# Performance work log

Hardware: AMD Instinct MI355X
Metric: run time of the kernel (lower is better)

The kernel has to match this reference:

```python
import jax, jax.numpy as jnp
import numpy as np

H = 16      # query heads
G = 4       # kv heads
D = 64      # head dim
ROPE_BASE = 10000.0

def _rotate_half(t):
    t1, t2 = jnp.split(t, 2, axis=-1)
    return jnp.concatenate([-t2, t1], axis=-1)

def _rope_emb(n):
    inv_freq = 1.0 / (ROPE_BASE ** (jnp.arange(0, D, 2, dtype=jnp.float32) / D))
    freqs = jnp.outer(jnp.arange(n, dtype=jnp.float32), inv_freq)  # [n, D/2]
    return jnp.concatenate([freqs, freqs], axis=-1)               # [n, D]

def setup_inputs() -> dict:
    key = jax.random.key(0)
    k1, k2, k3, k4 = jax.random.split(key, 4)
    B, N, C = 2, 2048, 1024
    x = jax.random.normal(k1, (B, N, C), dtype=jnp.float32)
    w_q = jax.random.normal(k2, (C, C), dtype=jnp.float32) * 0.02
    w_kv = jax.random.normal(k3, (C, 2 * G * D), dtype=jnp.float32) * 0.02
    w_out = jax.random.normal(k4, (C, C), dtype=jnp.float32) * 0.02
    return {"x": x, "w_q": w_q, "w_kv": w_kv, "w_out": w_out}

def reference(x, w_q, w_kv, w_out):
    B, N, C = x.shape
    scale = D ** -0.5
    q = (x @ w_q).reshape(B, N, H, D).transpose(0, 2, 1, 3)        # [B,H,N,D]
    kv = x @ w_kv
    k, v = jnp.split(kv, 2, axis=-1)
    k = k.reshape(B, N, G, D).transpose(0, 2, 1, 3)                # [B,G,N,D]
    v = v.reshape(B, N, G, D).transpose(0, 2, 1, 3)
    emb = _rope_emb(N)                                             # [N,D]
    cos, sin = jnp.cos(emb), jnp.sin(emb)
    q = q * cos + _rotate_half(q) * sin
    k = k * cos + _rotate_half(k) * sin
    # NOTE: faithful to source einsum -- kv-head axis g is SUMMED (absent from output)
    scores = jnp.einsum('bhid,bgjd->bhij', q, k) * scale           # [B,H,N,N]
    probs = jax.nn.softmax(scores, axis=-1)
    out = jnp.einsum('bhij,bgjd->bhid', probs, v)                  # [B,H,N,D]
    out = out.transpose(0, 2, 1, 3).reshape(B, N, H * D)
    return out @ w_out
```

## Files before the change

kernel.cpp:

```cpp
#include <hip/hip_runtime.h>
#include <hip/hip_bf16.h>
#include <math.h>

#define B_ 2
#define N_ 2048
#define C_ 1024
#define H_ 16
#define G_ 4
#define D_ 64
#define QKV_N 1152

using short8  = __attribute__((ext_vector_type(8))) short;
using short4v = __attribute__((ext_vector_type(4))) short;
using float4v = __attribute__((ext_vector_type(4))) float;

#if __has_builtin(__builtin_amdgcn_mfma_f32_16x16x16_bf16)
#define MFMA16K16(A, B, C) __builtin_amdgcn_mfma_f32_16x16x16_bf16(A, B, C, 0, 0, 0)
#else
#define MFMA16K16(A, B, C) __builtin_amdgcn_mfma_f32_16x16x16bf16_1k(A, B, C, 0, 0, 0)
#endif

__device__ __forceinline__ ushort f2bf(float f) {
    union { float f; unsigned u; } v; v.f = f;
    unsigned r = (v.u + 0x7FFF + ((v.u >> 16) & 1)) >> 16;
    return (ushort)r;
}
__device__ __forceinline__ float bf2f(ushort u) {
    union { unsigned u; float f; } t; t.u = ((unsigned)u) << 16; return t.f;
}
__device__ __forceinline__ unsigned pack_bf16(float a, float b) {
#if __has_builtin(__builtin_amdgcn_cvt_pk_bf16_f32)
    auto t = __builtin_amdgcn_cvt_pk_bf16_f32(a, b);
    unsigned r; __builtin_memcpy(&r, &t, 4); return r;
#else
    return (unsigned)f2bf(a) | ((unsigned)f2bf(b) << 16);
#endif
}
__device__ __forceinline__ float fexp2(float x) {
#if __has_builtin(__builtin_amdgcn_exp2f)
    return __builtin_amdgcn_exp2f(x);
#else
    return exp2f(x);
#endif
}

__device__ void tconv_body(const float* __restrict__ src, ushort* __restrict__ dst,
                           int K, int N, int bx, int by, float (*T)[65]) {
    const int n0 = bx * 64, k0 = by * 64;
    const int tid = threadIdx.x;
    #pragma unroll
    for (int s = 0; s < 16; ++s) {
        int idx = tid + s * 256; int r = idx >> 6, cc = idx & 63;
        T[r][cc] = src[(size_t)(k0 + r) * N + n0 + cc];
    }
    __syncthreads();
    #pragma unroll
    for (int s = 0; s < 16; ++s) {
        int idx = tid + s * 256; int r = idx >> 6, cc = idx & 63;
        dst[(size_t)(n0 + r) * K + k0 + cc] = f2bf(T[cc][r]);
    }
}

__global__ void prep(const float* __restrict__ x, const float* __restrict__ w_q,
                     const float* __restrict__ w_kv, const float* __restrict__ w_out,
                     ushort* __restrict__ xb, ushort* __restrict__ wqkvT,
                     ushort* __restrict__ woutT) {
    __shared__ float T[64][65];
    const int blk = blockIdx.x, tid = threadIdx.x;
    if (blk < 4096) {
        int i = blk * 1024 + tid * 4;
        float4 v = *(const float4*)(x + i);
        ushort4 o;
        o.x = f2bf(v.x); o.y = f2bf(v.y); o.z = f2bf(v.z); o.w = f2bf(v.w);
        *(ushort4*)(xb + i) = o;
    } else if (blk < 4352) {
        int idx = blk - 4096;
        tconv_body(w_q, wqkvT, C_, C_, idx & 15, idx >> 4, T);
    } else if (blk < 4608) {
        int idx = blk - 4352;
        tconv_body(w_out, woutT, C_, C_, idx & 15, idx >> 4, T);
    } else {
        const int k0 = (blk - 4608) * 64;
        #pragma unroll
        for (int it = 0; it < 4; ++it) {
            int p = tid + it * 256;
            int kk = p >> 4, d4 = (p & 15) * 4;
            float ks[4] = {0, 0, 0, 0}, vs[4] = {0, 0, 0, 0};
            #pragma unroll
            for (int g = 0; g < G_; ++g) {
                float4 a = *(const float4*)(w_kv + (size_t)(k0 + kk) * 512 + g * 64 + d4);
                float4 b = *(const float4*)(w_kv + (size_t)(k0 + kk) * 512 + 256 + g * 64 + d4);
                ks[0] += a.x; ks[1] += a.y; ks[2] += a.z; ks[3] += a.w;
                vs[0] += b.x; vs[1] += b.y; vs[2] += b.z; vs[3] += b.w;
            }
            #pragma unroll
            for (int e = 0; e < 4; ++e) {
                wqkvT[(size_t)(1024 + d4 + e) * C_ + k0 + kk] = f2bf(ks[e]);
                wqkvT[(size_t)(1088 + d4 + e) * C_ + k0 + kk] = f2bf(vs[e]);
            }
        }
    }
}

template <bool F32OUT>
__global__ __launch_bounds__(256) void gemm64(const ushort* __restrict__ A,
                                              const ushort* __restrict__ Bt,
                                              void* __restrict__ Cv,
                                              int M, int N, int K) {
    __shared__ __align__(16) ushort As[64 * 64];
    __shared__ __align__(16) ushort Bs[64 * 64];

    const int tid = threadIdx.x, wave = tid >> 6, lane = tid & 63;
    const int g = lane >> 4, c = lane & 15;
    const int wr = wave >> 1, wc = wave & 1;
    const int m0 = blockIdx.y * 64, n0 = blockIdx.x * 64;

    const int lr8 = lane >> 3, lq8 = lane & 7;
    const int gchunk = (lq8 ^ lr8) * 8;
    const ushort* pa = A  + (size_t)(m0 + wave * 16 + lr8) * K + gchunk;
    const ushort* pb = Bt + (size_t)(n0 + wave * 16 + lr8) * K + gchunk;

    float4v acc[2][2] = {{{0,0,0,0},{0,0,0,0}},{{0,0,0,0},{0,0,0,0}}};

    for (int k0 = 0; k0 < K; k0 += 64) {
        #pragma unroll
        for (int t = 0; t < 2; ++t) {
            __builtin_amdgcn_global_load_lds(
                (const __attribute__((address_space(1))) void*)(pa + (size_t)t * 8 * K + k0),
                (__attribute__((address_space(3))) void*)&As[(wave * 16 + t * 8) * 64], 16, 0, 0);
            __builtin_amdgcn_global_load_lds(
                (const __attribute__((address_space(1))) void*)(pb + (size_t)t * 8 * K + k0),
                (__attribute__((address_space(3))) void*)&Bs[(wave * 16 + t * 8) * 64], 16, 0, 0);
        }
        __syncthreads();

        #pragma unroll
        for (int kk = 0; kk < 2; ++kk) {
            const int c7 = c & 7;
            short8 af0 = *(const short8*)&As[(wr * 32 + c) * 64 + ((kk * 4 + g) ^ c7) * 8];
            short8 af1 = *(const short8*)&As[(wr * 32 + 16 + c) * 64 + ((kk * 4 + g) ^ c7) * 8];
            short8 bf0 = *(const short8*)&Bs[(wc * 32 + c) * 64 + ((kk * 4 + g) ^ c7) * 8];
            short8 bf1 = *(const short8*)&Bs[(wc * 32 + 16 + c) * 64 + ((kk * 4 + g) ^ c7) * 8];
            acc[0][0] = __builtin_amdgcn_mfma_f32_16x16x32_bf16(af0, bf0, acc[0][0], 0, 0, 0);
            acc[0][1] = __builtin_amdgcn_mfma_f32_16x16x32_bf16(af0, bf1, acc[0][1], 0, 0, 0);
            acc[1][0] = __builtin_amdgcn_mfma_f32_16x16x32_bf16(af1, bf0, acc[1][0], 0, 0, 0);
            acc[1][1] = __builtin_amdgcn_mfma_f32_16x16x32_bf16(af1, bf1, acc[1][1], 0, 0, 0);
        }
        __syncthreads();
    }

    #pragma unroll
    for (int a = 0; a < 2; ++a)
        #pragma unroll
        for (int bb = 0; bb < 2; ++bb)
            #pragma unroll
            for (int r = 0; r < 4; ++r) {
                int rowi = m0 + wr * 32 + a * 16 + 4 * g + r;
                int coli = n0 + wc * 32 + bb * 16 + c;
                if (F32OUT) ((float*)Cv)[(size_t)rowi * N + coli] = acc[a][bb][r];
                else ((ushort*)Cv)[(size_t)rowi * N + coli] = f2bf(acc[a][bb][r]);
            }
}

__global__ void rope_kv(const ushort* __restrict__ qkvb,
                        ushort* __restrict__ Kt, ushort* __restrict__ VtT) {
    const int wid = threadIdx.x >> 6, d = threadIdx.x & 63;
    const int rowg = blockIdx.x * 4 + wid;
    const int n = rowg & (N_ - 1), b = rowg >> 11;

    const ushort* base = qkvb + (size_t)rowg * QKV_N + 1024;
    float ks = bf2f(base[d]);
    float partner = __shfl_xor(ks, 32, 64);
    float rh = (d < 32) ? -partner : partner;
    float ang = (float)n * __powf(10000.0f, -(float)(d & 31) * (1.0f / 32.0f));
    float sn, cs; __sincosf(ang, &sn, &cs);

    Kt[(size_t)rowg * 64 + d] = f2bf(ks * cs + rh * sn);
    VtT[((size_t)b * 64 + d) * N_ + n] = base[64 + d];
}

#define QSCALE 0.18033688011112042f

__global__ __launch_bounds__(256) void attn9(
        const ushort* __restrict__ qkvb, const ushort* __restrict__ Kt,
        const ushort* __restrict__ VtT,
        ushort* __restrict__ oP0, ushort* __restrict__ oP1,
        float* __restrict__ lP0, float* __restrict__ lP1) {
    const int s  = blockIdx.x & 1;
    const int qt = (blockIdx.x >> 1) & 7;
    const int h  = (blockIdx.x >> 4) & 15;
    const int b  = blockIdx.x >> 8;
    const int tid = threadIdx.x, wave = tid >> 6, lane = tid & 63;
    const int g = lane >> 4, c = lane & 15;

    __shared__ __align__(16) ushort Ksh[64 * 64];
    __shared__ __align__(16) ushort Vsh[64 * 64];

    ushort* oPs = s ? oP1 : oP0;
    float*  lPs = s ? lP1 : lP0;

    const int i0 = qt * 256 + wave * 64;
    float invf[8];
    #pragma unroll
    for (int i = 0; i < 8; ++i)
        invf[i] = __powf(10000.0f, -(float)(8 * g + i) * (1.0f / 32.0f));

    short8 qf[4][2];
    #pragma unroll
    for (int a = 0; a < 4; ++a) {
        const int row = i0 + a * 16 + c;
        const ushort* qrow = qkvb + (size_t)(b * N_ + row) * QKV_N + h * 64;
        short8 raw0 = *(const short8*)(qrow + 8 * g);
        short8 raw1 = *(const short8*)(qrow + 32 + 8 * g);
        #pragma unroll
        for (int i = 0; i < 8; ++i) {
            float f0 = bf2f((ushort)raw0[i]), f1 = bf2f((ushort)raw1[i]);
            float sn, cs; __sincosf((float)row * invf[i], &sn, &cs);
            qf[a][0][i] = (short)f2bf((f0 * cs - f1 * sn) * QSCALE);
            qf[a][1][i] = (short)f2bf((f1 * cs + f0 * sn) * QSCALE);
        }
    }

    float4v o[4][4];
    #pragma unroll
    for (int a = 0; a < 4; ++a)
        #pragma unroll
        for (int f = 0; f < 4; ++f) o[a][f] = {0, 0, 0, 0};
    float ll[4] = {0.f, 0.f, 0.f, 0.f};

    const ushort* Kb = Kt  + (size_t)b * N_ * 64;
    const ushort* Vb = VtT + (size_t)b * 64 * N_;
    const int lr8 = lane >> 3, lq8 = lane & 7;
    const int wpos = (lq8 ^ lr8) * 8;
    const int j0 = s * (N_ / 2);
    const int NT = (N_ / 2) / 64;

    short8 kr0 = *(const short8*)(Kb + (size_t)(j0 + wave * 16 + lr8) * 64 + lq8 * 8);
    short8 kr1 = *(const short8*)(Kb + (size_t)(j0 + wave * 16 + 8 + lr8) * 64 + lq8 * 8);
    short8 vr0 = *(const short8*)(Vb + (size_t)(wave * 16 + lr8) * N_ + j0 + lq8 * 8);
    short8 vr1 = *(const short8*)(Vb + (size_t)(wave * 16 + 8 + lr8) * N_ + j0 + lq8 * 8);

    for (int t = 0; t < NT; ++t) {
        __syncthreads();
        *(short8*)&Ksh[(wave * 16 + lr8) * 64 + wpos]     = kr0;
        *(short8*)&Ksh[(wave * 16 + 8 + lr8) * 64 + wpos] = kr1;
        *(short8*)&Vsh[(wave * 16 + lr8) * 64 + wpos]     = vr0;
        *(short8*)&Vsh[(wave * 16 + 8 + lr8) * 64 + wpos] = vr1;
        __syncthreads();
        if (t + 1 < NT) {
            const int jn = j0 + (t + 1) * 64;
            kr0 = *(const short8*)(Kb + (size_t)(jn + wave * 16 + lr8) * 64 + lq8 * 8);
            kr1 = *(const short8*)(Kb + (size_t)(jn + wave * 16 + 8 + lr8) * 64 + lq8 * 8);
            vr0 = *(const short8*)(Vb + (size_t)(wave * 16 + lr8) * N_ + jn + lq8 * 8);
            vr1 = *(const short8*)(Vb + (size_t)(wave * 16 + 8 + lr8) * N_ + jn + lq8 * 8);
        }

        #pragma unroll
        for (int jt4 = 0; jt4 < 4; ++jt4) {
            const int R = jt4 * 16 + c;
            short8 kf0 = *(const short8*)&Ksh[R * 64 + ((g ^ (c & 7)) * 8)];
            short8 kf1 = *(const short8*)&Ksh[R * 64 + (((g ^ 4) ^ (c & 7)) * 8)];
            short4v vf[4];
            #pragma unroll
            for (int f = 0; f < 4; ++f)
                vf[f] = *(const short4v*)&Vsh[(16 * f + c) * 64 +
                          (((jt4 * 2 + (g >> 1)) ^ (c & 7)) * 8) + (g & 1) * 4];

            #pragma unroll
            for (int a = 0; a < 4; ++a) {
                float4v st = {0, 0, 0, 0};
                st = __builtin_amdgcn_mfma_f32_16x16x32_bf16(kf0, qf[a][0], st, 0, 0, 0);
                st = __builtin_amdgcn_mfma_f32_16x16x32_bf16(kf1, qf[a][1], st, 0, 0, 0);
                float p0 = fexp2(st[0]), p1 = fexp2(st[1]);
                float p2 = fexp2(st[2]), p3 = fexp2(st[3]);
                ll[a] += (p0 + p1) + (p2 + p3);
                union { unsigned u[2]; short4v v; } pk;
                pk.u[0] = pack_bf16(p0, p1);
                pk.u[1] = pack_bf16(p2, p3);
                #pragma unroll
                for (int f = 0; f < 4; ++f)
                    o[a][f] = MFMA16K16(vf[f], pk.v, o[a][f]);
            }
        }
    }

    #pragma unroll
    for (int a = 0; a < 4; ++a) {
        float lt = ll[a];
        lt += __shfl_xor(lt, 16, 64);
        lt += __shfl_xor(lt, 32, 64);
        const int row = i0 + a * 16 + c;
        if (g == 0) lPs[(size_t)(b * N_ + row) * 16 + h] = lt;
        #pragma unroll
        for (int f = 0; f < 4; ++f) {
            ushort4 w;
            w.x = f2bf(o[a][f][0]); w.y = f2bf(o[a][f][1]);
            w.z = f2bf(o[a][f][2]); w.w = f2bf(o[a][f][3]);
            *(ushort4*)(oPs + (size_t)(b * N_ + row) * 1024 + h * 64 + 16 * f + 4 * g) = w;
        }
    }
}

__global__ void combine(const ushort* __restrict__ oP0, const ushort* __restrict__ oP1,
                        const float* __restrict__ lP0, const float* __restrict__ lP1,
                        ushort* __restrict__ ao) {
    const int e = (blockIdx.x * 256 + threadIdx.x) * 4;
    const int row = e >> 10, hh = (e >> 6) & 15;
    const float inv = 1.0f / (lP0[row * 16 + hh] + lP1[row * 16 + hh]);
    ushort4 a = *(const ushort4*)(oP0 + e);
    ushort4 b = *(const ushort4*)(oP1 + e);
    ushort4 r;
    r.x = f2bf((bf2f(a.x) + bf2f(b.x)) * inv);
    r.y = f2bf((bf2f(a.y) + bf2f(b.y)) * inv);
    r.z = f2bf((bf2f(a.z) + bf2f(b.z)) * inv);
    r.w = f2bf((bf2f(a.w) + bf2f(b.w)) * inv);
    *(ushort4*)(ao + e) = r;
}

extern "C" void kernel_launch(void* const* d_in, const int* in_sizes, int n_in,
                              void* d_out, int out_size, void* d_ws, size_t ws_size,
                              hipStream_t stream) {
    const float* x     = (const float*)d_in[0];
    const float* w_q   = (const float*)d_in[1];
    const float* w_kv  = (const float*)d_in[2];
    const float* w_out = (const float*)d_in[3];
    float* out = (float*)d_out;

    const int M = B_ * N_;
    ushort* xb    = (ushort*)d_ws;
    ushort* wqkvT = xb    + (size_t)M * C_;
    ushort* woutT = wqkvT + (size_t)QKV_N * C_;
    ushort* qkvb  = woutT + (size_t)C_ * C_;
    ushort* Kt    = qkvb  + (size_t)M * QKV_N;
    ushort* VtT   = Kt    + (size_t)B_ * N_ * D_;
    ushort* oP1   = VtT   + (size_t)B_ * D_ * N_;
    float*  lP0   = (float*)(oP1 + (size_t)M * C_);
    float*  lP1   = lP0 + (size_t)M * H_;
    ushort* oP0   = xb;
    ushort* ao    = xb;

    prep<<<4624, 256, 0, stream>>>(x, w_q, w_kv, w_out, xb, wqkvT, woutT);
    gemm64<false><<<dim3(QKV_N / 64, M / 64), 256, 0, stream>>>(xb, wqkvT, qkvb, M, QKV_N, C_);
    rope_kv<<<M / 4, 256, 0, stream>>>(qkvb, Kt, VtT);
    attn9<<<B_ * H_ * (N_ / 256) * 2, 256, 0, stream>>>(qkvb, Kt, VtT, oP0, oP1, lP0, lP1);
    combine<<<(M * C_) / 1024, 256, 0, stream>>>(oP0, oP1, lP0, lP1, ao);
    gemm64<true><<<dim3(C_ / 64, M / 64), 256, 0, stream>>>(ao, woutT, out, M, C_, C_);
}
```

Baseline: 181.2 us.

## Enlarge GEMM tile to 128x64 and halve attention query tile per block

The projection GEMMs now use a 128x64 block tile, with each wave computing a 32x64 strip from 2x4 MFMA fragments. This raises arithmetic intensity per LDS load and halves the number of blocks. The attention kernel now processes 128 query rows per block (32 per wave) instead of 256, which doubles the grid and cuts per-wave accumulator registers, with launch bounds requesting 4 blocks per CU. The attention change trades more K/V reloads per query for higher occupancy and better load balance across CUs.

```diff
diff --git a/kernel.cpp b/kernel.cpp
--- a/kernel.cpp
+++ b/kernel.cpp
@@ -103,62 +103,71 @@
 }
 
 template <bool F32OUT>
-__global__ __launch_bounds__(256) void gemm64(const ushort* __restrict__ A,
-                                              const ushort* __restrict__ Bt,
-                                              void* __restrict__ Cv,
-                                              int M, int N, int K) {
-    __shared__ __align__(16) ushort As[64 * 64];
+__global__ __launch_bounds__(256, 4) void gemm128(const ushort* __restrict__ A,
+                                                  const ushort* __restrict__ Bt,
+                                                  void* __restrict__ Cv,
+                                                  int M, int N, int K) {
+    __shared__ __align__(16) ushort As[128 * 64];
     __shared__ __align__(16) ushort Bs[64 * 64];
 
     const int tid = threadIdx.x, wave = tid >> 6, lane = tid & 63;
     const int g = lane >> 4, c = lane & 15;
-    const int wr = wave >> 1, wc = wave & 1;
-    const int m0 = blockIdx.y * 64, n0 = blockIdx.x * 64;
-
-    const int lr8 = lane >> 3, lq8 = lane & 7;
-    const int gchunk = (lq8 ^ lr8) * 8;
-    const ushort* pa = A  + (size_t)(m0 + wave * 16 + lr8) * K + gchunk;
-    const ushort* pb = Bt + (size_t)(n0 + wave * 16 + lr8) * K + gchunk;
-
-    float4v acc[2][2] = {{{0,0,0,0},{0,0,0,0}},{{0,0,0,0},{0,0,0,0}}};
+    const int m0 = blockIdx.y * 128, n0 = blockIdx.x * 64;
+
+    const int lr = tid >> 3;
+    const int lq = tid & 7;
+    const int gsw = (lq ^ (lr & 7)) * 8;
+    const ushort* pa = A  + (size_t)(m0 + lr) * K + gsw;
+    const ushort* pb = Bt + (size_t)(n0 + lr) * K + gsw;
+
+    float4v acc[2][4];
+    #pragma unroll
+    for (int m = 0; m < 2; ++m)
+        #pragma unroll
+        for (int n = 0; n < 4; ++n) acc[m][n] = {0, 0, 0, 0};
 
     for (int k0 = 0; k0 < K; k0 += 64) {
         #pragma unroll
-        for (int t = 0; t < 2; ++t) {
+        for (int i = 0; i < 4; ++i)
             __builtin_amdgcn_global_load_lds(
-                (const __attribute__((address_space(1))) void*)(pa + (size_t)t * 8 * K + k0),
-                (__attribute__((address_space(3))) void*)&As[(wave * 16 + t * 8) * 64], 16, 0, 0);
+                (const __attribute__((address_space(1))) void*)(pa + (size_t)i * 32 * K + k0),
+                (__attribute__((address_space(3))) void*)&As[(i * 32 + wave * 8) * 64], 16, 0, 0);
+        #pragma unroll
+        for (int i = 0; i < 2; ++i)
             __builtin_amdgcn_global_load_lds(
-                (const __attribute__((address_space(1))) void*)(pb + (size_t)t * 8 * K + k0),
-                (__attribute__((address_space(3))) void*)&Bs[(wave * 16 + t * 8) * 64], 16, 0, 0);
-        }
+                (const __attribute__((address_space(1))) void*)(pb + (size_t)i * 32 * K + k0),
+                (__attribute__((address_space(3))) void*)&Bs[(i * 32 + wave * 8) * 64], 16, 0, 0);
         __syncthreads();
 
         #pragma unroll
         for (int kk = 0; kk < 2; ++kk) {
             const int c7 = c & 7;
-            short8 af0 = *(const short8*)&As[(wr * 32 + c) * 64 + ((kk * 4 + g) ^ c7) * 8];
-            short8 af1 = *(const short8*)&As[(wr * 32 + 16 + c) * 64 + ((kk * 4 + g) ^ c7) * 8];
-            short8 bf0 = *(const short8*)&Bs[(wc * 32 + c) * 64 + ((kk * 4 + g) ^ c7) * 8];
-            short8 bf1 = *(const short8*)&Bs[(wc * 32 + 16 + c) * 64 + ((kk * 4 + g) ^ c7) * 8];
-            acc[0][0] = __builtin_amdgcn_mfma_f32_16x16x32_bf16(af0, bf0, acc[0][0], 0, 0, 0);
-            acc[0][1] = __builtin_amdgcn_mfma_f32_16x16x32_bf16(af0, bf1, acc[0][1], 0, 0, 0);
-            acc[1][0] = __builtin_amdgcn_mfma_f32_16x16x32_bf16(af1, bf0, acc[1][0], 0, 0, 0);
-            acc[1][1] = __builtin_amdgcn_mfma_f32_16x16x32_bf16(af1, bf1, acc[1][1], 0, 0, 0);
+            short8 af[2], bf[4];
+            #pragma unroll
+            for (int m = 0; m < 2; ++m)
+                af[m] = *(const short8*)&As[(wave * 32 + m * 16 + c) * 64 + ((kk * 4 + g) ^ c7) * 8];
+            #pragma unroll
+            for (int n = 0; n < 4; ++n)
+                bf[n] = *(const short8*)&Bs[(n * 16 + c) * 64 + ((kk * 4 + g) ^ c7) * 8];
+            #pragma unroll
+            for (int m = 0; m < 2; ++m)
+                #pragma unroll
+                for (int n = 0; n < 4; ++n)
+                    acc[m][n] = __builtin_amdgcn_mfma_f32_16x16x32_bf16(af[m], bf[n], acc[m][n], 0, 0, 0);
         }
         __syncthreads();
     }
 
     #pragma unroll
-    for (int a = 0; a < 2; ++a)
-        #pragma unroll
-        for (int bb = 0; bb < 2; ++bb)
+    for (int m = 0; m < 2; ++m)
+        #pragma unroll
+        for (int n = 0; n < 4; ++n)
             #pragma unroll
             for (int r = 0; r < 4; ++r) {
-                int rowi = m0 + wr * 32 + a * 16 + 4 * g + r;
-                int coli = n0 + wc * 32 + bb * 16 + c;
-                if (F32OUT) ((float*)Cv)[(size_t)rowi * N + coli] = acc[a][bb][r];
-                else ((ushort*)Cv)[(size_t)rowi * N + coli] = f2bf(acc[a][bb][r]);
+                int rowi = m0 + wave * 32 + m * 16 + 4 * g + r;
+                int coli = n0 + n * 16 + c;
+                if (F32OUT) ((float*)Cv)[(size_t)rowi * N + coli] = acc[m][n][r];
+                else ((ushort*)Cv)[(size_t)rowi * N + coli] = f2bf(acc[m][n][r]);
             }
 }
 
@@ -181,15 +190,15 @@
 
 #define QSCALE 0.18033688011112042f
 
-__global__ __launch_bounds__(256) void attn9(
+__global__ __launch_bounds__(256, 4) void attn10(
         const ushort* __restrict__ qkvb, const ushort* __restrict__ Kt,
         const ushort* __restrict__ VtT,
         ushort* __restrict__ oP0, ushort* __restrict__ oP1,
         float* __restrict__ lP0, float* __restrict__ lP1) {
     const int s  = blockIdx.x & 1;
-    const int qt = (blockIdx.x >> 1) & 7;
-    const int h  = (blockIdx.x >> 4) & 15;
-    const int b  = blockIdx.x >> 8;
+    const int qt = (blockIdx.x >> 1) & 15;
+    const int h  = (blockIdx.x >> 5) & 15;
+    const int b  = blockIdx.x >> 9;
     const int tid = threadIdx.x, wave = tid >> 6, lane = tid & 63;
     const int g = lane >> 4, c = lane & 15;
 
@@ -199,15 +208,15 @@
     ushort* oPs = s ? oP1 : oP0;
     float*  lPs = s ? lP1 : lP0;
 
-    const int i0 = qt * 256 + wave * 64;
+    const int i0 = qt * 128 + wave * 32;
     float invf[8];
     #pragma unroll
     for (int i = 0; i < 8; ++i)
         invf[i] = __powf(10000.0f, -(float)(8 * g + i) * (1.0f / 32.0f));
 
-    short8 qf[4][2];
-    #pragma unroll
-    for (int a = 0; a < 4; ++a) {
+    short8 qf[2][2];
+    #pragma unroll
+    for (int a = 0; a < 2; ++a) {
         const int row = i0 + a * 16 + c;
         const ushort* qrow = qkvb + (size_t)(b * N_ + row) * QKV_N + h * 64;
         short8 raw0 = *(const short8*)(qrow + 8 * g);
@@ -221,12 +230,12 @@
         }
     }
 
-    float4v o[4][4];
-    #pragma unroll
-    for (int a = 0; a < 4; ++a)
+    float4v o[2][4];
+    #pragma unroll
+    for (int a = 0; a < 2; ++a)
         #pragma unroll
         for (int f = 0; f < 4; ++f) o[a][f] = {0, 0, 0, 0};
-    float ll[4] = {0.f, 0.f, 0.f, 0.f};
+    float ll[2] = {0.f, 0.f};
 
     const ushort* Kb = Kt  + (size_t)b * N_ * 64;
     const ushort* Vb = VtT + (size_t)b * 64 * N_;
@@ -267,7 +276,7 @@
                           (((jt4 * 2 + (g >> 1)) ^ (c & 7)) * 8) + (g & 1) * 4];
 
             #pragma unroll
-            for (int a = 0; a < 4; ++a) {
+            for (int a = 0; a < 2; ++a) {
                 float4v st = {0, 0, 0, 0};
                 st = __builtin_amdgcn_mfma_f32_16x16x32_bf16(kf0, qf[a][0], st, 0, 0, 0);
                 st = __builtin_amdgcn_mfma_f32_16x16x32_bf16(kf1, qf[a][1], st, 0, 0, 0);
@@ -285,7 +294,7 @@
     }
 
     #pragma unroll
-    for (int a = 0; a < 4; ++a) {
+    for (int a = 0; a < 2; ++a) {
         float lt = ll[a];
         lt += __shfl_xor(lt, 16, 64);
         lt += __shfl_xor(lt, 32, 64);
@@ -340,9 +349,9 @@
     ushort* ao    = xb;
 
     prep<<<4624, 256, 0, stream>>>(x, w_q, w_kv, w_out, xb, wqkvT, woutT);
-    gemm64<false><<<dim3(QKV_N / 64, M / 64), 256, 0, stream>>>(xb, wqkvT, qkvb, M, QKV_N, C_);
+    gemm128<false><<<dim3(QKV_N / 64, M / 128), 256, 0, stream>>>(xb, wqkvT, qkvb, M, QKV_N, C_);
     rope_kv<<<M / 4, 256, 0, stream>>>(qkvb, Kt, VtT);
-    attn9<<<B_ * H_ * (N_ / 256) * 2, 256, 0, stream>>>(qkvb, Kt, VtT, oP0, oP1, lP0, lP1);
+    attn10<<<B_ * H_ * (N_ / 128) * 2, 256, 0, stream>>>(qkvb, Kt, VtT, oP0, oP1, lP0, lP1);
     combine<<<(M * C_) / 1024, 256, 0, stream>>>(oP0, oP1, lP0, lP1, ao);
-    gemm64<true><<<dim3(C_ / 64, M / 64), 256, 0, stream>>>(ao, woutT, out, M, C_, C_);
-}
+    gemm128<true><<<dim3(C_ / 64, M / 128), 256, 0, stream>>>(ao, woutT, out, M, C_, C_);
+}
```

Result: slower. 190.1 us (+4.9%).
